# Optimization experiments

Hardware: AMD Instinct MI355X
Metric: run time of the kernel (lower is better)

## Reference

```python
import jax, jax.numpy as jnp
import numpy as np

D = 96

def setup_inputs() -> dict:
    key = jax.random.key(0)
    ks = jax.random.split(key, 7)
    B, S = 8, 4096
    scale = 1.0 / np.sqrt(D)
    return {
        "h": jax.random.normal(ks[0], (B, S, D), dtype=jnp.float32),
        "Wq": jax.random.normal(ks[1], (D, D), dtype=jnp.float32) * scale,
        "bq": jnp.zeros((D,), dtype=jnp.float32),
        "Wk": jax.random.normal(ks[2], (D, D), dtype=jnp.float32) * scale,
        "bk": jnp.zeros((D,), dtype=jnp.float32),
        "Wv": jax.random.normal(ks[3], (D, D), dtype=jnp.float32) * scale,
        "bv": jnp.zeros((D,), dtype=jnp.float32),
    }

def reference(h, Wq, bq, Wk, bk, Wv, bv):
    # torch Linear: x @ W.T + b
    Q = jnp.einsum('bsd,ed->bse', h, Wq) + bq
    K = jnp.einsum('bsd,ed->bse', h, Wk) + bk
    V = jnp.einsum('bsd,ed->bse', h, Wv) + bv
    scores = jnp.einsum('bse,bte->bst', Q, K) / jnp.sqrt(jnp.float32(D))
    attn = jax.nn.softmax(scores, axis=-1)  # [B,S,S]
    return jnp.einsum('bst,bte->bse', attn, V)
```

## Files before the change

### kernel.cpp

```cpp
#include <hip/hip_runtime.h>

typedef float f32x16 __attribute__((ext_vector_type(16)));
typedef __bf16 bf16x8 __attribute__((ext_vector_type(8)));
typedef const void __attribute__((address_space(1)))* gas_t;
typedef void __attribute__((address_space(3)))* las_t;

__device__ __forceinline__ unsigned short f2bf(float x) {
  union { __bf16 b; unsigned short u; } c; c.b = (__bf16)x; return c.u;
}
__device__ __forceinline__ unsigned pk2(float a, float b) {
  union { __bf16 h[2]; unsigned u; } c;
  c.h[0] = (__bf16)a; c.h[1] = (__bf16)b;
  return c.u;
}
__device__ __forceinline__ float bflo(unsigned u) { return __uint_as_float(u << 16); }
__device__ __forceinline__ float bfhi(unsigned u) { return __uint_as_float(u & 0xffff0000u); }

__global__ __launch_bounds__(256) void qkv_kernel(
    const float* __restrict__ h,
    const float* __restrict__ Wq, const float* __restrict__ bq,
    const float* __restrict__ Wk, const float* __restrict__ bk,
    const float* __restrict__ Wv, const float* __restrict__ bv,
    unsigned short* __restrict__ Qb, unsigned short* __restrict__ Kb,
    unsigned short* __restrict__ Vt)
{
  __shared__ char sm[128*192 + 3*96*192];
  char* Hsh = sm;
  char* Wsh = sm + 128*192;
  const int tid = threadIdx.x;
  const int blk = blockIdx.x;

  #pragma unroll
  for (int i = 0; i < 12; ++i) {
    int idx = tid + 256*i;
    int row = idx / 24, c4 = idx % 24;
    float4 v = *(const float4*)(h + ((size_t)blk*128 + row)*96 + c4*4);
    uint2 pk;
    pk.x = pk2(v.x, v.y);
    pk.y = pk2(v.z, v.w);
    *(uint2*)(Hsh + ((row*192 + c4*8) ^ ((row & 7) << 4))) = pk;
  }
  const float* Ws[3] = {Wq, Wk, Wv};
  #pragma unroll 1
  for (int w = 0; w < 3; ++w) {
    const float* W = Ws[w];
    #pragma unroll
    for (int i = 0; i < 9; ++i) {
      int idx = tid + 256*i;
      int row = idx / 24, c4 = idx % 24;
      float4 v = *(const float4*)(W + row*96 + c4*4);
      uint2 pk;
      pk.x = pk2(v.x, v.y);
      pk.y = pk2(v.z, v.w);
      *(uint2*)(Wsh + w*18432 + ((row*192 + c4*8) ^ ((row & 7) << 4))) = pk;
    }
  }
  __syncthreads();

  const int lane = tid & 63, wv = tid >> 6, hi = lane >> 5, ln = lane & 31;
  const int mrow0 = wv * 32;

  bf16x8 af[6];
  #pragma unroll
  for (int c = 0; c < 6; ++c)
    af[c] = *(const bf16x8*)(Hsh + (((mrow0 + ln)*192 + c*32 + hi*16) ^ ((ln & 7) << 4)));

  const float* biases[3] = {bq, bk, bv};
  #pragma unroll 1
  for (int w = 0; w < 3; ++w) {
    f32x16 acc[3];
    #pragma unroll
    for (int j = 0; j < 3; ++j)
      #pragma unroll
      for (int r = 0; r < 16; ++r) acc[j][r] = 0.f;

    #pragma unroll
    for (int c = 0; c < 6; ++c) {
      #pragma unroll
      for (int j = 0; j < 3; ++j) {
        bf16x8 bfr = *(const bf16x8*)(Wsh + w*18432 +
                      (((ln + 32*j)*192 + c*32 + hi*16) ^ ((ln & 7) << 4)));
        acc[j] = __builtin_amdgcn_mfma_f32_32x32x16_bf16(af[c], bfr, acc[j], 0, 0, 0);
      }
    }
    #pragma unroll
    for (int j = 0; j < 3; ++j) {
      const int e = ln + 32*j;
      const float bias = biases[w][e];
      if (w == 2) {
        #pragma unroll
        for (int g = 0; g < 4; ++g) {
          int srow = blk*128 + mrow0 + 8*g + 4*hi;
          int sperm = (srow & ~12) | ((srow & 4) << 1) | ((srow & 8) >> 1);
          int b = sperm >> 12, s = sperm & 4095;
          uint2 pk;
          pk.x = pk2(acc[j][4*g+0] + bias, acc[j][4*g+1] + bias);
          pk.y = pk2(acc[j][4*g+2] + bias, acc[j][4*g+3] + bias);
          *(uint2*)(Vt + ((size_t)b*96 + e)*4096 + s) = pk;
        }
      } else {
        unsigned short* Outp = (w == 0) ? Qb : Kb;
        const float sc = (w == 0) ? 0.14724443849485857f : 1.0f;
        #pragma unroll
        for (int r = 0; r < 16; ++r) {
          int grow = blk*128 + mrow0 + (r & 3) + 8*(r >> 2) + 4*hi;
          Outp[(size_t)grow*96 + e] = f2bf((acc[j][r] + bias) * sc);
        }
      }
    }
  }
}

__global__ __launch_bounds__(256, 2) void flash_kernel(
    const unsigned short* __restrict__ Qb, const unsigned short* __restrict__ Kb,
    const unsigned short* __restrict__ Vt, unsigned short* __restrict__ Opb,
    float* __restrict__ ml, int NT)
{
  __shared__ char sm[2*12288];
  const int tid = threadIdx.x;
  const int lane = tid & 63, wv = tid >> 6, hi = lane >> 5, ln = lane & 31;
  const int qt = blockIdx.x, bb = blockIdx.y, sp = blockIdx.z;
  const int q0 = qt*256 + wv*64;
  const size_t qrowA = (size_t)bb*4096 + q0 + ln;
  const size_t qrowB = qrowA + 32;
  const int sbase = sp * (NT*32);

  const unsigned short* qp = Qb + qrowA*96 + hi*8;

  const unsigned short* Kbase = Kb + ((size_t)bb*4096 + sbase)*96;
  const unsigned short* Vbase = Vt + (size_t)bb*96*4096 + sbase;

  int ksrcA, ksrcB;
  {
    int d = tid*16;
    int r = d / 192;
    int u = d ^ ((r & 7) << 4);
    if (u / 192 != r) { r = u / 192; u = d ^ ((r & 7) << 4); }
    ksrcA = r*96 + ((u - r*192) >> 1);
    d = (256 + tid)*16;
    r = d / 192;
    u = d ^ ((r & 7) << 4);
    if (u / 192 != r) { r = u / 192; u = d ^ ((r & 7) << 4); }
    ksrcB = r*96 + ((u - r*192) >> 1);
  }
  int vsrcA, vsrcB;
  {
    int d = tid*16;
    int u = d ^ ((((d >> 6) >> 1) & 7) << 4);
    int e = u >> 6;
    vsrcA = e*4096 + ((u & 63) >> 1);
    d = (256 + tid)*16;
    u = d ^ ((((d >> 6) >> 1) & 7) << 4);
    e = u >> 6;
    vsrcB = e*4096 + ((u & 63) >> 1);
  }

  {
    __builtin_amdgcn_global_load_lds((gas_t)(const void*)(Kbase + ksrcA),
                                     (las_t)(void*)(sm + wv*1024), 16, 0, 0);
    __builtin_amdgcn_global_load_lds((gas_t)(const void*)(Vbase + vsrcA),
                                     (las_t)(void*)(sm + 6144 + wv*1024), 16, 0, 0);
    if (tid < 128) {
      __builtin_amdgcn_global_load_lds((gas_t)(const void*)(Kbase + ksrcB),
                                       (las_t)(void*)(sm + 4096 + wv*1024), 16, 0, 0);
      __builtin_amdgcn_global_load_lds((gas_t)(const void*)(Vbase + vsrcB),
                                       (las_t)(void*)(sm + 6144 + 4096 + wv*1024), 16, 0, 0);
    }
  }
  __syncthreads();

  f32x16 accA[3], accB[3];
  #pragma unroll
  for (int j = 0; j < 3; ++j)
    #pragma unroll
    for (int r = 0; r < 16; ++r) { accA[j][r] = 0.f; accB[j][r] = 0.f; }

  float lA = 0.f, lB = 0.f;

  for (int st = 0; st < NT; ++st) {
    char* B  = sm + (st & 1)*12288;
    char* Bn = sm + ((st & 1) ^ 1)*12288;

    if (st + 1 < NT) {
      const unsigned short* Kt = Kbase + (st + 1)*32*96;
      const unsigned short* Vp = Vbase + (st + 1)*32;
      __builtin_amdgcn_global_load_lds((gas_t)(const void*)(Kt + ksrcA),
                                       (las_t)(void*)(Bn + wv*1024), 16, 0, 0);
      __builtin_amdgcn_global_load_lds((gas_t)(const void*)(Vp + vsrcA),
                                       (las_t)(void*)(Bn + 6144 + wv*1024), 16, 0, 0);
      if (tid < 128) {
        __builtin_amdgcn_global_load_lds((gas_t)(const void*)(Kt + ksrcB),
                                         (las_t)(void*)(Bn + 4096 + wv*1024), 16, 0, 0);
        __builtin_amdgcn_global_load_lds((gas_t)(const void*)(Vp + vsrcB),
                                         (las_t)(void*)(Bn + 6144 + 4096 + wv*1024), 16, 0, 0);
      }
    }

    f32x16 sA, sB;
    #pragma unroll
    for (int r = 0; r < 16; ++r) { sA[r] = 0.f; sB[r] = 0.f; }
    __builtin_amdgcn_s_setprio(1);
    #pragma unroll
    for (int c = 0; c < 6; ++c) {
      bf16x8 k0 = *(const bf16x8*)(B + ((ln*192 + c*32 + hi*16) ^ ((ln & 7) << 4)));
      bf16x8 qa = *(const bf16x8*)(qp + c*16);
      bf16x8 qb = *(const bf16x8*)(qp + 32*96 + c*16);
      sA = __builtin_amdgcn_mfma_f32_32x32x16_bf16(k0, qa, sA, 0, 0, 0);
      sB = __builtin_amdgcn_mfma_f32_32x32x16_bf16(k0, qb, sB, 0, 0, 0);
    }
    __builtin_amdgcn_s_setprio(0);

    #pragma unroll
    for (int r = 0; r < 16; ++r) { sA[r] = __builtin_amdgcn_exp2f(sA[r]); }
    #pragma unroll
    for (int r = 0; r < 16; ++r) { sB[r] = __builtin_amdgcn_exp2f(sB[r]); }
    {
      float t0 = 0.f, t1 = 0.f, u0 = 0.f, u1 = 0.f;
      #pragma unroll
      for (int r = 0; r < 8; ++r) {
        t0 += sA[r]; t1 += sA[r + 8];
        u0 += sB[r]; u1 += sB[r + 8];
      }
      lA += t0 + t1;
      lB += u0 + u1;
    }

    bf16x8 pfA[2], pfB[2];
    #pragma unroll
    for (int c1 = 0; c1 < 2; ++c1) {
      union { bf16x8 v; unsigned u[4]; } fa, fb;
      #pragma unroll
      for (int k = 0; k < 4; ++k) {
        fa.u[k] = pk2(sA[c1*8 + 2*k], sA[c1*8 + 2*k + 1]);
        fb.u[k] = pk2(sB[c1*8 + 2*k], sB[c1*8 + 2*k + 1]);
      }
      pfA[c1] = fa.v; pfB[c1] = fb.v;
    }

    __builtin_amdgcn_s_setprio(1);
    #pragma unroll
    for (int c1 = 0; c1 < 2; ++c1) {
      #pragma unroll
      for (int j = 0; j < 3; ++j) {
        const int e = ln + 32*j;
        bf16x8 vf = *(const bf16x8*)(B + 6144 +
                      ((e*64 + c1*32 + hi*16) ^ (((e >> 1) & 7) << 4)));
        accA[j] = __builtin_amdgcn_mfma_f32_32x32x16_bf16(vf, pfA[c1], accA[j], 0, 0, 0);
        accB[j] = __builtin_amdgcn_mfma_f32_32x32x16_bf16(vf, pfB[c1], accB[j], 0, 0, 0);
      }
    }
    __builtin_amdgcn_s_setprio(0);

    __syncthreads();
  }

  lA += __shfl_xor(lA, 32, 64);
  lB += __shfl_xor(lB, 32, 64);
  unsigned short* OrowA = Opb + ((size_t)sp*3145728 + qrowA*96);
  unsigned short* OrowB = Opb + ((size_t)sp*3145728 + qrowB*96);
  #pragma unroll
  for (int j = 0; j < 3; ++j)
    #pragma unroll
    for (int g = 0; g < 4; ++g) {
      uint2 oa, ob;
      oa.x = pk2(accA[j][4*g+0], accA[j][4*g+1]);
      oa.y = pk2(accA[j][4*g+2], accA[j][4*g+3]);
      ob.x = pk2(accB[j][4*g+0], accB[j][4*g+1]);
      ob.y = pk2(accB[j][4*g+2], accB[j][4*g+3]);
      *(uint2*)(OrowA + 32*j + 8*g + 4*hi) = oa;
      *(uint2*)(OrowB + 32*j + 8*g + 4*hi) = ob;
    }
  if (hi == 0) {
    ml[(size_t)sp*32768 + qrowA] = lA;
    ml[(size_t)sp*32768 + qrowB] = lB;
  }
}

__global__ __launch_bounds__(256) void combine_kernel(
    const unsigned short* __restrict__ Opb, const float* __restrict__ ml,
    float* __restrict__ out)
{
  const int g = blockIdx.x*256 + threadIdx.x;
  const int row = g / 12, e8 = (g % 12) * 8;
  float ls = 0.f;
  #pragma unroll
  for (int s = 0; s < 4; ++s) ls += ml[(size_t)s*32768 + row];
  const float inv = 1.0f / ls;
  float acc[8] = {0.f, 0.f, 0.f, 0.f, 0.f, 0.f, 0.f, 0.f};
  #pragma unroll
  for (int s = 0; s < 4; ++s) {
    uint4 d = *(const uint4*)(Opb + (size_t)s*3145728 + (size_t)row*96 + e8);
    acc[0] += bflo(d.x); acc[1] += bfhi(d.x);
    acc[2] += bflo(d.y); acc[3] += bfhi(d.y);
    acc[4] += bflo(d.z); acc[5] += bfhi(d.z);
    acc[6] += bflo(d.w); acc[7] += bfhi(d.w);
  }
  float4 o0 = make_float4(acc[0]*inv, acc[1]*inv, acc[2]*inv, acc[3]*inv);
  float4 o1 = make_float4(acc[4]*inv, acc[5]*inv, acc[6]*inv, acc[7]*inv);
  float* po = out + (size_t)row*96 + e8;
  *(float4*)(po) = o0;
  *(float4*)(po + 4) = o1;
}

extern "C" void kernel_launch(void* const* d_in, const int* in_sizes, int n_in,
                              void* d_out, int out_size, void* d_ws, size_t ws_size,
                              hipStream_t stream) {
  const float* h  = (const float*)d_in[0];
  const float* Wq = (const float*)d_in[1];
  const float* bq = (const float*)d_in[2];
  const float* Wk = (const float*)d_in[3];
  const float* bk = (const float*)d_in[4];
  const float* Wv = (const float*)d_in[5];
  const float* bv = (const float*)d_in[6];
  float* out = (float*)d_out;
  char* ws = (char*)d_ws;
  unsigned short* Qb  = (unsigned short*)(ws);
  unsigned short* Kb  = (unsigned short*)(ws + 6291456);
  unsigned short* Vt  = (unsigned short*)(ws + 12582912);
  unsigned short* Opb = (unsigned short*)(ws + 18874368);
  float*          mlp = (float*)(ws + 44040192);

  qkv_kernel<<<256, 256, 0, stream>>>(h, Wq, bq, Wk, bk, Wv, bv, Qb, Kb, Vt);
  flash_kernel<<<dim3(16, 8, 4), 256, 0, stream>>>(Qb, Kb, Vt, Opb, mlp, 32);
  combine_kernel<<<1536, 256, 0, stream>>>(Opb, mlp, out);
}
```

Before: 88.11 us.

## Halve per-wave query rows and read V directly from global memory

Each wave now handles 32 query rows instead of 64, so the grid doubles to 32x8x4 blocks and per-thread accumulator registers are halved. V tiles are no longer staged through LDS; each wave loads its V fragments straight from global memory, which shrinks shared memory to the K double buffer only. The intent is higher occupancy and less LDS traffic. In exchange, K is reused across fewer query rows, and the global V reads sit on the critical path without prefetching.

```diff
diff --git a/kernel.cpp b/kernel.cpp
--- a/kernel.cpp
+++ b/kernel.cpp
@@ -116,16 +116,15 @@
     const unsigned short* __restrict__ Vt, unsigned short* __restrict__ Opb,
     float* __restrict__ ml, int NT)
 {
-  __shared__ char sm[2*12288];
+  __shared__ char sm[2*6144];
   const int tid = threadIdx.x;
   const int lane = tid & 63, wv = tid >> 6, hi = lane >> 5, ln = lane & 31;
   const int qt = blockIdx.x, bb = blockIdx.y, sp = blockIdx.z;
-  const int q0 = qt*256 + wv*64;
-  const size_t qrowA = (size_t)bb*4096 + q0 + ln;
-  const size_t qrowB = qrowA + 32;
+  const int q0 = qt*128 + wv*32;
+  const size_t qrow = (size_t)bb*4096 + q0 + ln;
   const int sbase = sp * (NT*32);
 
-  const unsigned short* qp = Qb + qrowA*96 + hi*8;
+  const unsigned short* qp = Qb + qrow*96 + hi*8;
 
   const unsigned short* Kbase = Kb + ((size_t)bb*4096 + sbase)*96;
   const unsigned short* Vbase = Vt + (size_t)bb*96*4096 + sbase;
@@ -143,136 +142,100 @@
     if (u / 192 != r) { r = u / 192; u = d ^ ((r & 7) << 4); }
     ksrcB = r*96 + ((u - r*192) >> 1);
   }
-  int vsrcA, vsrcB;
-  {
-    int d = tid*16;
-    int u = d ^ ((((d >> 6) >> 1) & 7) << 4);
-    int e = u >> 6;
-    vsrcA = e*4096 + ((u & 63) >> 1);
-    d = (256 + tid)*16;
-    u = d ^ ((((d >> 6) >> 1) & 7) << 4);
-    e = u >> 6;
-    vsrcB = e*4096 + ((u & 63) >> 1);
-  }
+
+  int voff[3];
+  #pragma unroll
+  for (int j = 0; j < 3; ++j) voff[j] = (ln + 32*j)*4096 + hi*8;
 
   {
     __builtin_amdgcn_global_load_lds((gas_t)(const void*)(Kbase + ksrcA),
                                      (las_t)(void*)(sm + wv*1024), 16, 0, 0);
-    __builtin_amdgcn_global_load_lds((gas_t)(const void*)(Vbase + vsrcA),
-                                     (las_t)(void*)(sm + 6144 + wv*1024), 16, 0, 0);
-    if (tid < 128) {
+    if (tid < 128)
       __builtin_amdgcn_global_load_lds((gas_t)(const void*)(Kbase + ksrcB),
                                        (las_t)(void*)(sm + 4096 + wv*1024), 16, 0, 0);
-      __builtin_amdgcn_global_load_lds((gas_t)(const void*)(Vbase + vsrcB),
-                                       (las_t)(void*)(sm + 6144 + 4096 + wv*1024), 16, 0, 0);
-    }
   }
   __syncthreads();
 
-  f32x16 accA[3], accB[3];
+  f32x16 accO[3];
   #pragma unroll
   for (int j = 0; j < 3; ++j)
     #pragma unroll
-    for (int r = 0; r < 16; ++r) { accA[j][r] = 0.f; accB[j][r] = 0.f; }
-
-  float lA = 0.f, lB = 0.f;
+    for (int r = 0; r < 16; ++r) accO[j][r] = 0.f;
+
+  float l = 0.f;
 
   for (int st = 0; st < NT; ++st) {
-    char* B  = sm + (st & 1)*12288;
-    char* Bn = sm + ((st & 1) ^ 1)*12288;
+    char* B  = sm + (st & 1)*6144;
+    char* Bn = sm + ((st & 1) ^ 1)*6144;
 
     if (st + 1 < NT) {
       const unsigned short* Kt = Kbase + (st + 1)*32*96;
-      const unsigned short* Vp = Vbase + (st + 1)*32;
       __builtin_amdgcn_global_load_lds((gas_t)(const void*)(Kt + ksrcA),
                                        (las_t)(void*)(Bn + wv*1024), 16, 0, 0);
-      __builtin_amdgcn_global_load_lds((gas_t)(const void*)(Vp + vsrcA),
-                                       (las_t)(void*)(Bn + 6144 + wv*1024), 16, 0, 0);
-      if (tid < 128) {
+      if (tid < 128)
         __builtin_amdgcn_global_load_lds((gas_t)(const void*)(Kt + ksrcB),
                                          (las_t)(void*)(Bn + 4096 + wv*1024), 16, 0, 0);
-        __builtin_amdgcn_global_load_lds((gas_t)(const void*)(Vp + vsrcB),
-                                         (las_t)(void*)(Bn + 6144 + 4096 + wv*1024), 16, 0, 0);
+    }
+
+    f32x16 s;
+    #pragma unroll
+    for (int r = 0; r < 16; ++r) s[r] = 0.f;
+    __builtin_amdgcn_s_setprio(1);
+    #pragma unroll
+    for (int c = 0; c < 6; ++c) {
+      bf16x8 qa = *(const bf16x8*)(qp + c*16);
+      bf16x8 k0 = *(const bf16x8*)(B + ((ln*192 + c*32 + hi*16) ^ ((ln & 7) << 4)));
+      s = __builtin_amdgcn_mfma_f32_32x32x16_bf16(k0, qa, s, 0, 0, 0);
+    }
+    __builtin_amdgcn_s_setprio(0);
+
+    #pragma unroll
+    for (int r = 0; r < 16; ++r) { s[r] = __builtin_amdgcn_exp2f(s[r]); }
+    {
+      float t0 = 0.f, t1 = 0.f;
+      #pragma unroll
+      for (int r = 0; r < 8; ++r) { t0 += s[r]; t1 += s[r + 8]; }
+      l += t0 + t1;
+    }
+
+    bf16x8 pf[2];
+    #pragma unroll
+    for (int c1 = 0; c1 < 2; ++c1) {
+      union { bf16x8 v; unsigned u[4]; } f;
+      #pragma unroll
+      for (int k = 0; k < 4; ++k)
+        f.u[k] = pk2(s[c1*8 + 2*k], s[c1*8 + 2*k + 1]);
+      pf[c1] = f.v;
+    }
+
+    const unsigned short* Vst = Vbase + st*32;
+    __builtin_amdgcn_s_setprio(1);
+    #pragma unroll
+    for (int c1 = 0; c1 < 2; ++c1) {
+      #pragma unroll
+      for (int j = 0; j < 3; ++j) {
+        bf16x8 vf = *(const bf16x8*)(Vst + voff[j] + c1*16);
+        accO[j] = __builtin_amdgcn_mfma_f32_32x32x16_bf16(vf, pf[c1], accO[j], 0, 0, 0);
       }
     }
-
-    f32x16 sA, sB;
-    #pragma unroll
-    for (int r = 0; r < 16; ++r) { sA[r] = 0.f; sB[r] = 0.f; }
-    __builtin_amdgcn_s_setprio(1);
-    #pragma unroll
-    for (int c = 0; c < 6; ++c) {
-      bf16x8 k0 = *(const bf16x8*)(B + ((ln*192 + c*32 + hi*16) ^ ((ln & 7) << 4)));
-      bf16x8 qa = *(const bf16x8*)(qp + c*16);
-      bf16x8 qb = *(const bf16x8*)(qp + 32*96 + c*16);
-      sA = __builtin_amdgcn_mfma_f32_32x32x16_bf16(k0, qa, sA, 0, 0, 0);
-      sB = __builtin_amdgcn_mfma_f32_32x32x16_bf16(k0, qb, sB, 0, 0, 0);
-    }
     __builtin_amdgcn_s_setprio(0);
 
-    #pragma unroll
-    for (int r = 0; r < 16; ++r) { sA[r] = __builtin_amdgcn_exp2f(sA[r]); }
-    #pragma unroll
-    for (int r = 0; r < 16; ++r) { sB[r] = __builtin_amdgcn_exp2f(sB[r]); }
-    {
-      float t0 = 0.f, t1 = 0.f, u0 = 0.f, u1 = 0.f;
-      #pragma unroll
-      for (int r = 0; r < 8; ++r) {
-        t0 += sA[r]; t1 += sA[r + 8];
-        u0 += sB[r]; u1 += sB[r + 8];
-      }
-      lA += t0 + t1;
-      lB += u0 + u1;
-    }
-
-    bf16x8 pfA[2], pfB[2];
-    #pragma unroll
-    for (int c1 = 0; c1 < 2; ++c1) {
-      union { bf16x8 v; unsigned u[4]; } fa, fb;
-      #pragma unroll
-      for (int k = 0; k < 4; ++k) {
-        fa.u[k] = pk2(sA[c1*8 + 2*k], sA[c1*8 + 2*k + 1]);
-        fb.u[k] = pk2(sB[c1*8 + 2*k], sB[c1*8 + 2*k + 1]);
-      }
-      pfA[c1] = fa.v; pfB[c1] = fb.v;
-    }
-
-    __builtin_amdgcn_s_setprio(1);
-    #pragma unroll
-    for (int c1 = 0; c1 < 2; ++c1) {
-      #pragma unroll
-      for (int j = 0; j < 3; ++j) {
-        const int e = ln + 32*j;
-        bf16x8 vf = *(const bf16x8*)(B + 6144 +
-                      ((e*64 + c1*32 + hi*16) ^ (((e >> 1) & 7) << 4)));
-        accA[j] = __builtin_amdgcn_mfma_f32_32x32x16_bf16(vf, pfA[c1], accA[j], 0, 0, 0);
-        accB[j] = __builtin_amdgcn_mfma_f32_32x32x16_bf16(vf, pfB[c1], accB[j], 0, 0, 0);
-      }
-    }
-    __builtin_amdgcn_s_setprio(0);
-
     __syncthreads();
   }
 
-  lA += __shfl_xor(lA, 32, 64);
-  lB += __shfl_xor(lB, 32, 64);
-  unsigned short* OrowA = Opb + ((size_t)sp*3145728 + qrowA*96);
-  unsigned short* OrowB = Opb + ((size_t)sp*3145728 + qrowB*96);
+  l += __shfl_xor(l, 32, 64);
+  unsigned short* Orow = Opb + ((size_t)sp*3145728 + qrow*96);
   #pragma unroll
   for (int j = 0; j < 3; ++j)
     #pragma unroll
     for (int g = 0; g < 4; ++g) {
-      uint2 oa, ob;
-      oa.x = pk2(accA[j][4*g+0], accA[j][4*g+1]);
-      oa.y = pk2(accA[j][4*g+2], accA[j][4*g+3]);
-      ob.x = pk2(accB[j][4*g+0], accB[j][4*g+1]);
-      ob.y = pk2(accB[j][4*g+2], accB[j][4*g+3]);
-      *(uint2*)(OrowA + 32*j + 8*g + 4*hi) = oa;
-      *(uint2*)(OrowB + 32*j + 8*g + 4*hi) = ob;
+      uint2 oa;
+      oa.x = pk2(accO[j][4*g+0], accO[j][4*g+1]);
+      oa.y = pk2(accO[j][4*g+2], accO[j][4*g+3]);
+      *(uint2*)(Orow + 32*j + 8*g + 4*hi) = oa;
     }
   if (hi == 0) {
-    ml[(size_t)sp*32768 + qrowA] = lA;
-    ml[(size_t)sp*32768 + qrowB] = lB;
+    ml[(size_t)sp*32768 + qrow] = l;
   }
 }
 
@@ -321,6 +284,6 @@
   float*          mlp = (float*)(ws + 44040192);
 
   qkv_kernel<<<256, 256, 0, stream>>>(h, Wq, bq, Wk, bk, Wv, bv, Qb, Kb, Vt);
-  flash_kernel<<<dim3(16, 8, 4), 256, 0, stream>>>(Qb, Kb, Vt, Opb, mlp, 32);
+  flash_kernel<<<dim3(32, 8, 4), 256, 0, stream>>>(Qb, Kb, Vt, Opb, mlp, 32);
   combine_kernel<<<1536, 256, 0, stream>>>(Opb, mlp, out);
 }
```

Result: slower. 134.9 us (+53.1%).

## Split QKV projection across grid and double flash K/V tile per barrier

Applied to the files above, without the earlier changes.

The QKV projection kernel now launches one block per (row tile, weight) with a 2D grid instead of looping over three weights in one block. This triples parallelism and cuts shared memory per block, at the cost of reloading and converting the h tile three times. The flash kernel now stages 64 keys per iteration (two 32-key subtiles) into double-buffered LDS and halves the loop count. This halves the number of barriers and async-load rounds but doubles the LDS footprint to 48KB.

```diff
diff --git a/kernel.cpp b/kernel.cpp
--- a/kernel.cpp
+++ b/kernel.cpp
@@ -24,11 +24,14 @@
     unsigned short* __restrict__ Qb, unsigned short* __restrict__ Kb,
     unsigned short* __restrict__ Vt)
 {
-  __shared__ char sm[128*192 + 3*96*192];
+  __shared__ char sm[128*192 + 96*192];
   char* Hsh = sm;
   char* Wsh = sm + 128*192;
   const int tid = threadIdx.x;
   const int blk = blockIdx.x;
+  const int w = blockIdx.y;
+  const float* W    = (w == 0) ? Wq : (w == 1) ? Wk : Wv;
+  const float* bias = (w == 0) ? bq : (w == 1) ? bk : bv;
 
   #pragma unroll
   for (int i = 0; i < 12; ++i) {
@@ -40,72 +43,59 @@
     pk.y = pk2(v.z, v.w);
     *(uint2*)(Hsh + ((row*192 + c4*8) ^ ((row & 7) << 4))) = pk;
   }
-  const float* Ws[3] = {Wq, Wk, Wv};
-  #pragma unroll 1
-  for (int w = 0; w < 3; ++w) {
-    const float* W = Ws[w];
-    #pragma unroll
-    for (int i = 0; i < 9; ++i) {
-      int idx = tid + 256*i;
-      int row = idx / 24, c4 = idx % 24;
-      float4 v = *(const float4*)(W + row*96 + c4*4);
-      uint2 pk;
-      pk.x = pk2(v.x, v.y);
-      pk.y = pk2(v.z, v.w);
-      *(uint2*)(Wsh + w*18432 + ((row*192 + c4*8) ^ ((row & 7) << 4))) = pk;
-    }
+  #pragma unroll
+  for (int i = 0; i < 9; ++i) {
+    int idx = tid + 256*i;
+    int row = idx / 24, c4 = idx % 24;
+    float4 v = *(const float4*)(W + row*96 + c4*4);
+    uint2 pk;
+    pk.x = pk2(v.x, v.y);
+    pk.y = pk2(v.z, v.w);
+    *(uint2*)(Wsh + ((row*192 + c4*8) ^ ((row & 7) << 4))) = pk;
   }
   __syncthreads();
 
   const int lane = tid & 63, wv = tid >> 6, hi = lane >> 5, ln = lane & 31;
   const int mrow0 = wv * 32;
 
-  bf16x8 af[6];
-  #pragma unroll
-  for (int c = 0; c < 6; ++c)
-    af[c] = *(const bf16x8*)(Hsh + (((mrow0 + ln)*192 + c*32 + hi*16) ^ ((ln & 7) << 4)));
-
-  const float* biases[3] = {bq, bk, bv};
-  #pragma unroll 1
-  for (int w = 0; w < 3; ++w) {
-    f32x16 acc[3];
-    #pragma unroll
-    for (int j = 0; j < 3; ++j)
-      #pragma unroll
-      for (int r = 0; r < 16; ++r) acc[j][r] = 0.f;
-
-    #pragma unroll
-    for (int c = 0; c < 6; ++c) {
-      #pragma unroll
-      for (int j = 0; j < 3; ++j) {
-        bf16x8 bfr = *(const bf16x8*)(Wsh + w*18432 +
-                      (((ln + 32*j)*192 + c*32 + hi*16) ^ ((ln & 7) << 4)));
-        acc[j] = __builtin_amdgcn_mfma_f32_32x32x16_bf16(af[c], bfr, acc[j], 0, 0, 0);
-      }
-    }
+  f32x16 acc[3];
+  #pragma unroll
+  for (int j = 0; j < 3; ++j)
+    #pragma unroll
+    for (int r = 0; r < 16; ++r) acc[j][r] = 0.f;
+
+  #pragma unroll
+  for (int c = 0; c < 6; ++c) {
+    bf16x8 af = *(const bf16x8*)(Hsh + (((mrow0 + ln)*192 + c*32 + hi*16) ^ ((ln & 7) << 4)));
     #pragma unroll
     for (int j = 0; j < 3; ++j) {
-      const int e = ln + 32*j;
-      const float bias = biases[w][e];
-      if (w == 2) {
-        #pragma unroll
-        for (int g = 0; g < 4; ++g) {
-          int srow = blk*128 + mrow0 + 8*g + 4*hi;
-          int sperm = (srow & ~12) | ((srow & 4) << 1) | ((srow & 8) >> 1);
-          int b = sperm >> 12, s = sperm & 4095;
-          uint2 pk;
-          pk.x = pk2(acc[j][4*g+0] + bias, acc[j][4*g+1] + bias);
-          pk.y = pk2(acc[j][4*g+2] + bias, acc[j][4*g+3] + bias);
-          *(uint2*)(Vt + ((size_t)b*96 + e)*4096 + s) = pk;
-        }
-      } else {
-        unsigned short* Outp = (w == 0) ? Qb : Kb;
-        const float sc = (w == 0) ? 0.14724443849485857f : 1.0f;
-        #pragma unroll
-        for (int r = 0; r < 16; ++r) {
-          int grow = blk*128 + mrow0 + (r & 3) + 8*(r >> 2) + 4*hi;
-          Outp[(size_t)grow*96 + e] = f2bf((acc[j][r] + bias) * sc);
-        }
+      bf16x8 bfr = *(const bf16x8*)(Wsh +
+                    (((ln + 32*j)*192 + c*32 + hi*16) ^ ((ln & 7) << 4)));
+      acc[j] = __builtin_amdgcn_mfma_f32_32x32x16_bf16(af, bfr, acc[j], 0, 0, 0);
+    }
+  }
+  #pragma unroll
+  for (int j = 0; j < 3; ++j) {
+    const int e = ln + 32*j;
+    const float b = bias[e];
+    if (w == 2) {
+      #pragma unroll
+      for (int g = 0; g < 4; ++g) {
+        int srow = blk*128 + mrow0 + 8*g + 4*hi;
+        int sperm = (srow & ~12) | ((srow & 4) << 1) | ((srow & 8) >> 1);
+        int bb = sperm >> 12, s = sperm & 4095;
+        uint2 pk;
+        pk.x = pk2(acc[j][4*g+0] + b, acc[j][4*g+1] + b);
+        pk.y = pk2(acc[j][4*g+2] + b, acc[j][4*g+3] + b);
+        *(uint2*)(Vt + ((size_t)bb*96 + e)*4096 + s) = pk;
+      }
+    } else {
+      unsigned short* Outp = (w == 0) ? Qb : Kb;
+      const float sc = (w == 0) ? 0.14724443849485857f : 1.0f;
+      #pragma unroll
+      for (int r = 0; r < 16; ++r) {
+        int grow = blk*128 + mrow0 + (r & 3) + 8*(r >> 2) + 4*hi;
+        Outp[(size_t)grow*96 + e] = f2bf((acc[j][r] + b) * sc);
       }
     }
   }
@@ -116,56 +106,44 @@
     const unsigned short* __restrict__ Vt, unsigned short* __restrict__ Opb,
     float* __restrict__ ml, int NT)
 {
-  __shared__ char sm[2*12288];
+  __shared__ char sm[2*24576];
   const int tid = threadIdx.x;
   const int lane = tid & 63, wv = tid >> 6, hi = lane >> 5, ln = lane & 31;
   const int qt = blockIdx.x, bb = blockIdx.y, sp = blockIdx.z;
   const int q0 = qt*256 + wv*64;
   const size_t qrowA = (size_t)bb*4096 + q0 + ln;
   const size_t qrowB = qrowA + 32;
-  const int sbase = sp * (NT*32);
+  const int sbase = sp * (NT*64);
 
   const unsigned short* qp = Qb + qrowA*96 + hi*8;
 
   const unsigned short* Kbase = Kb + ((size_t)bb*4096 + sbase)*96;
   const unsigned short* Vbase = Vt + (size_t)bb*96*4096 + sbase;
 
-  int ksrcA, ksrcB;
-  {
-    int d = tid*16;
+  int ksrc[3], vsrc[3], kdst[3];
+  #pragma unroll
+  for (int i = 0; i < 3; ++i) {
+    int sub, d;
+    if (i == 0)      { sub = 0; d = tid*16; }
+    else if (i == 1) { sub = (tid < 128) ? 0 : 1;
+                       d = (tid < 128) ? (tid + 256)*16 : (tid - 128)*16; }
+    else             { sub = 1; d = (tid + 128)*16; }
     int r = d / 192;
     int u = d ^ ((r & 7) << 4);
     if (u / 192 != r) { r = u / 192; u = d ^ ((r & 7) << 4); }
-    ksrcA = r*96 + ((u - r*192) >> 1);
-    d = (256 + tid)*16;
-    r = d / 192;
-    u = d ^ ((r & 7) << 4);
-    if (u / 192 != r) { r = u / 192; u = d ^ ((r & 7) << 4); }
-    ksrcB = r*96 + ((u - r*192) >> 1);
-  }
-  int vsrcA, vsrcB;
-  {
-    int d = tid*16;
-    int u = d ^ ((((d >> 6) >> 1) & 7) << 4);
-    int e = u >> 6;
-    vsrcA = e*4096 + ((u & 63) >> 1);
-    d = (256 + tid)*16;
-    u = d ^ ((((d >> 6) >> 1) & 7) << 4);
-    e = u >> 6;
-    vsrcB = e*4096 + ((u & 63) >> 1);
-  }
-
-  {
-    __builtin_amdgcn_global_load_lds((gas_t)(const void*)(Kbase + ksrcA),
-                                     (las_t)(void*)(sm + wv*1024), 16, 0, 0);
-    __builtin_amdgcn_global_load_lds((gas_t)(const void*)(Vbase + vsrcA),
-                                     (las_t)(void*)(sm + 6144 + wv*1024), 16, 0, 0);
-    if (tid < 128) {
-      __builtin_amdgcn_global_load_lds((gas_t)(const void*)(Kbase + ksrcB),
-                                       (las_t)(void*)(sm + 4096 + wv*1024), 16, 0, 0);
-      __builtin_amdgcn_global_load_lds((gas_t)(const void*)(Vbase + vsrcB),
-                                       (las_t)(void*)(sm + 6144 + 4096 + wv*1024), 16, 0, 0);
-    }
+    ksrc[i] = sub*32*96 + r*96 + ((u - r*192) >> 1);
+    int uv = d ^ ((((d >> 6) >> 1) & 7) << 4);
+    int e = uv >> 6;
+    vsrc[i] = sub*32 + e*4096 + ((uv & 63) >> 1);
+    kdst[i] = sub*12288 + d;
+  }
+
+  #pragma unroll
+  for (int i = 0; i < 3; ++i) {
+    __builtin_amdgcn_global_load_lds((gas_t)(const void*)(Kbase + ksrc[i]),
+                                     (las_t)(void*)(sm + kdst[i]), 16, 0, 0);
+    __builtin_amdgcn_global_load_lds((gas_t)(const void*)(Vbase + vsrc[i]),
+                                     (las_t)(void*)(sm + kdst[i] + 6144), 16, 0, 0);
   }
   __syncthreads();
 
@@ -178,78 +156,81 @@
   float lA = 0.f, lB = 0.f;
 
   for (int st = 0; st < NT; ++st) {
-    char* B  = sm + (st & 1)*12288;
-    char* Bn = sm + ((st & 1) ^ 1)*12288;
+    char* B  = sm + (st & 1)*24576;
+    char* Bn = sm + ((st & 1) ^ 1)*24576;
 
     if (st + 1 < NT) {
-      const unsigned short* Kt = Kbase + (st + 1)*32*96;
-      const unsigned short* Vp = Vbase + (st + 1)*32;
-      __builtin_amdgcn_global_load_lds((gas_t)(const void*)(Kt + ksrcA),
-                                       (las_t)(void*)(Bn + wv*1024), 16, 0, 0);
-      __builtin_amdgcn_global_load_lds((gas_t)(const void*)(Vp + vsrcA),
-                                       (las_t)(void*)(Bn + 6144 + wv*1024), 16, 0, 0);
-      if (tid < 128) {
-        __builtin_amdgcn_global_load_lds((gas_t)(const void*)(Kt + ksrcB),
-                                         (las_t)(void*)(Bn + 4096 + wv*1024), 16, 0, 0);
-        __builtin_amdgcn_global_load_lds((gas_t)(const void*)(Vp + vsrcB),
-                                         (las_t)(void*)(Bn + 6144 + 4096 + wv*1024), 16, 0, 0);
-      }
-    }
-
-    f32x16 sA, sB;
-    #pragma unroll
-    for (int r = 0; r < 16; ++r) { sA[r] = 0.f; sB[r] = 0.f; }
-    __builtin_amdgcn_s_setprio(1);
-    #pragma unroll
-    for (int c = 0; c < 6; ++c) {
-      bf16x8 k0 = *(const bf16x8*)(B + ((ln*192 + c*32 + hi*16) ^ ((ln & 7) << 4)));
-      bf16x8 qa = *(const bf16x8*)(qp + c*16);
-      bf16x8 qb = *(const bf16x8*)(qp + 32*96 + c*16);
-      sA = __builtin_amdgcn_mfma_f32_32x32x16_bf16(k0, qa, sA, 0, 0, 0);
-      sB = __builtin_amdgcn_mfma_f32_32x32x16_bf16(k0, qb, sB, 0, 0, 0);
-    }
-    __builtin_amdgcn_s_setprio(0);
-
-    #pragma unroll
-    for (int r = 0; r < 16; ++r) { sA[r] = __builtin_amdgcn_exp2f(sA[r]); }
-    #pragma unroll
-    for (int r = 0; r < 16; ++r) { sB[r] = __builtin_amdgcn_exp2f(sB[r]); }
-    {
-      float t0 = 0.f, t1 = 0.f, u0 = 0.f, u1 = 0.f;
-      #pragma unroll
-      for (int r = 0; r < 8; ++r) {
-        t0 += sA[r]; t1 += sA[r + 8];
-        u0 += sB[r]; u1 += sB[r + 8];
-      }
-      lA += t0 + t1;
-      lB += u0 + u1;
-    }
-
-    bf16x8 pfA[2], pfB[2];
-    #pragma unroll
-    for (int c1 = 0; c1 < 2; ++c1) {
-      union { bf16x8 v; unsigned u[4]; } fa, fb;
-      #pragma unroll
-      for (int k = 0; k < 4; ++k) {
-        fa.u[k] = pk2(sA[c1*8 + 2*k], sA[c1*8 + 2*k + 1]);
-        fb.u[k] = pk2(sB[c1*8 + 2*k], sB[c1*8 + 2*k + 1]);
-      }
-      pfA[c1] = fa.v; pfB[c1] = fb.v;
-    }
-
-    __builtin_amdgcn_s_setprio(1);
-    #pragma unroll
-    for (int c1 = 0; c1 < 2; ++c1) {
-      #pragma unroll
-      for (int j = 0; j < 3; ++j) {
-        const int e = ln + 32*j;
-        bf16x8 vf = *(const bf16x8*)(B + 6144 +
-                      ((e*64 + c1*32 + hi*16) ^ (((e >> 1) & 7) << 4)));
-        accA[j] = __builtin_amdgcn_mfma_f32_32x32x16_bf16(vf, pfA[c1], accA[j], 0, 0, 0);
-        accB[j] = __builtin_amdgcn_mfma_f32_32x32x16_bf16(vf, pfB[c1], accB[j], 0, 0, 0);
-      }
-    }
-    __builtin_amdgcn_s_setprio(0);
+      const unsigned short* Kt = Kbase + (st + 1)*64*96;
+      const unsigned short* Vp = Vbase + (st + 1)*64;
+      #pragma unroll
+      for (int i = 0; i < 3; ++i) {
+        __builtin_amdgcn_global_load_lds((gas_t)(const void*)(Kt + ksrc[i]),
+                                         (las_t)(void*)(Bn + kdst[i]), 16, 0, 0);
+        __builtin_amdgcn_global_load_lds((gas_t)(const void*)(Vp + vsrc[i]),
+                                         (las_t)(void*)(Bn + kdst[i] + 6144), 16, 0, 0);
+      }
+    }
+
+    #pragma unroll
+    for (int sub = 0; sub < 2; ++sub) {
+      char* Ks = B + sub*12288;
+      char* Vs = Ks + 6144;
+
+      f32x16 sA, sB;
+      #pragma unroll
+      for (int r = 0; r < 16; ++r) { sA[r] = 0.f; sB[r] = 0.f; }
+      __builtin_amdgcn_s_setprio(1);
+      #pragma unroll
+      for (int c = 0; c < 6; ++c) {
+        bf16x8 k0 = *(const bf16x8*)(Ks + ((ln*192 + c*32 + hi*16) ^ ((ln & 7) << 4)));
+        bf16x8 qa = *(const bf16x8*)(qp + c*16);
+        bf16x8 qb = *(const bf16x8*)(qp + 32*96 + c*16);
+        sA = __builtin_amdgcn_mfma_f32_32x32x16_bf16(k0, qa, sA, 0, 0, 0);
+        sB = __builtin_amdgcn_mfma_f32_32x32x16_bf16(k0, qb, sB, 0, 0, 0);
+      }
+      __builtin_amdgcn_s_setprio(0);
+
+      #pragma unroll
+      for (int r = 0; r < 16; ++r) { sA[r] = __builtin_amdgcn_exp2f(sA[r]); }
+      #pragma unroll
+      for (int r = 0; r < 16; ++r) { sB[r] = __builtin_amdgcn_exp2f(sB[r]); }
+      {
+        float t0 = 0.f, t1 = 0.f, u0 = 0.f, u1 = 0.f;
+        #pragma unroll
+        for (int r = 0; r < 8; ++r) {
+          t0 += sA[r]; t1 += sA[r + 8];
+          u0 += sB[r]; u1 += sB[r + 8];
+        }
+        lA += t0 + t1;
+        lB += u0 + u1;
+      }
+
+      bf16x8 pfA[2], pfB[2];
+      #pragma unroll
+      for (int c1 = 0; c1 < 2; ++c1) {
+        union { bf16x8 v; unsigned u[4]; } fa, fb;
+        #pragma unroll
+        for (int k = 0; k < 4; ++k) {
+          fa.u[k] = pk2(sA[c1*8 + 2*k], sA[c1*8 + 2*k + 1]);
+          fb.u[k] = pk2(sB[c1*8 + 2*k], sB[c1*8 + 2*k + 1]);
+        }
+        pfA[c1] = fa.v; pfB[c1] = fb.v;
+      }
+
+      __builtin_amdgcn_s_setprio(1);
+      #pragma unroll
+      for (int c1 = 0; c1 < 2; ++c1) {
+        #pragma unroll
+        for (int j = 0; j < 3; ++j) {
+          const int e = ln + 32*j;
+          bf16x8 vf = *(const bf16x8*)(Vs +
+                        ((e*64 + c1*32 + hi*16) ^ (((e >> 1) & 7) << 4)));
+          accA[j] = __builtin_amdgcn_mfma_f32_32x32x16_bf16(vf, pfA[c1], accA[j], 0, 0, 0);
+          accB[j] = __builtin_amdgcn_mfma_f32_32x32x16_bf16(vf, pfB[c1], accB[j], 0, 0, 0);
+        }
+      }
+      __builtin_amdgcn_s_setprio(0);
+    }
 
     __syncthreads();
   }
@@ -320,7 +301,7 @@
   unsigned short* Opb = (unsigned short*)(ws + 18874368);
   float*          mlp = (float*)(ws + 44040192);
 
-  qkv_kernel<<<256, 256, 0, stream>>>(h, Wq, bq, Wk, bk, Wv, bv, Qb, Kb, Vt);
-  flash_kernel<<<dim3(16, 8, 4), 256, 0, stream>>>(Qb, Kb, Vt, Opb, mlp, 32);
+  qkv_kernel<<<dim3(256, 3), 256, 0, stream>>>(h, Wq, bq, Wk, bk, Wv, bv, Qb, Kb, Vt);
+  flash_kernel<<<dim3(16, 8, 4), 256, 0, stream>>>(Qb, Kb, Vt, Opb, mlp, 16);
   combine_kernel<<<1536, 256, 0, stream>>>(Opb, mlp, out);
 }
```

After: 113.5 us. 1.29x slower.
